# Optimization experiments

Hardware: AMD Instinct MI355X
Metric: run time of the kernel (lower is better)

The kernel has to match this reference:

```python
import jax, jax.numpy as jnp
import numpy as np

N, E, IN, H = 20000, 50000, 32, 64


def _lin_init(k, fan_in, shape):
    b = 1.0 / np.sqrt(fan_in)
    return jax.random.uniform(k, shape, jnp.float32, -b, b)


def setup_inputs() -> dict:
    key = jax.random.key(0)
    ks = jax.random.split(key, 16)
    inp = {
        "x": jax.random.normal(ks[0], (N, IN), jnp.float32),
        "edge_index": jax.random.randint(ks[1], (2, E), 0, N, dtype=jnp.int32),
        "edge_attr": jax.random.normal(ks[2], (E, 1, 2), jnp.float32),
        # layer 0: edge MLP 2->H->IN*H, root [IN,H], bias [H]
        "w1_0": _lin_init(ks[3], 2, (2, H)),
        "b1_0": _lin_init(ks[4], 2, (H,)),
        "w2_0": _lin_init(ks[5], H, (H, IN * H)),
        "b2_0": _lin_init(ks[6], H, (IN * H,)),
        "root_0": _lin_init(ks[7], IN, (IN, H)),
        "bias_0": _lin_init(ks[8], IN, (H,)),
        # layer 1: edge MLP 2->H->H*H, root [H,H], bias [H]
        "w1_1": _lin_init(ks[9], 2, (2, H)),
        "b1_1": _lin_init(ks[10], 2, (H,)),
        "w2_1": _lin_init(ks[11], H, (H, H * H)),
        "b2_1": _lin_init(ks[12], H, (H * H,)),
        "root_1": _lin_init(ks[13], H, (H, H)),
        "bias_1": _lin_init(ks[14], H, (H,)),
    }
    return inp


def _nnconv(x, src, dst, ea, w1, b1, w2, b2, root, bias, in_c, out_c):
    # per-edge weight matrices from edge-attr MLP: [E, in_c*out_c]
    h = jax.nn.relu(ea @ w1 + b1) @ w2 + b2
    W = h.reshape(-1, in_c, out_c)                     # [E, in, out]
    msg = jnp.einsum('ei,eio->eo', x[src], W)          # gather + per-edge matmul
    agg = jax.ops.segment_sum(msg, dst, num_segments=x.shape[0])  # scatter-add
    return agg + x @ root + bias                       # add aggr (PyG NNConv, aggr='add')


def reference(x, edge_index, edge_attr,
              w1_0, b1_0, w2_0, b2_0, root_0, bias_0,
              w1_1, b1_1, w2_1, b2_1, root_1, bias_1):
    src, dst = edge_index[0], edge_index[1]
    ea = edge_attr.reshape(edge_attr.shape[0], 2)      # [E, 2]
    x = jax.nn.relu(_nnconv(x, src, dst, ea, w1_0, b1_0, w2_0, b2_0, root_0, bias_0, IN, H))
    x = jax.nn.relu(_nnconv(x, src, dst, ea, w1_1, b1_1, w2_1, b2_1, root_1, bias_1, H, H))
    return x
```

## Files before the change

### kernel.cpp

```cpp
#include <hip/hip_runtime.h>

typedef _Float16 v8h __attribute__((ext_vector_type(8)));
typedef float v16f __attribute__((ext_vector_type(16)));

__global__ void prep_fused(const float* __restrict__ w2_0, const float* __restrict__ b2_0,
                           _Float16* __restrict__ BF0,
                           const float* __restrict__ w2_1, const float* __restrict__ b2_1,
                           _Float16* __restrict__ BF1,
                           const float* __restrict__ x, const float* __restrict__ root,
                           const float* __restrict__ bias, float* __restrict__ agg,
                           _Float16* __restrict__ xb, int N) {
    int idx = blockIdx.x * 256 + threadIdx.x;
    const int n0 = 264 * 512;
    const int n1 = 528 * 512;
    if (idx < n0 + n1) {
        const float* w2; const float* b2; _Float16* BF; int IN, rel;
        if (idx < n0) { w2 = w2_0; b2 = b2_0; BF = BF0; IN = 32; rel = idx; }
        else          { w2 = w2_1; b2 = b2_1; BF = BF1; IN = 64; rel = idx - n0; }
        int j = rel & 7, lane = (rel >> 3) & 63, f = rel >> 9;
        int nf = f & 1, kk16 = f >> 1;
        int ln = lane & 31, g2 = lane >> 5;
        int k = kk16 * 16 + g2 * 8 + j;
        int ko = k / IN, i = k - ko * IN;
        int o = nf * 32 + ln;
        float v = (ko < 64) ? w2[ko * (IN * 64) + i * 64 + o]
                : (ko == 64 ? b2[i * 64 + o] : 0.f);
        BF[rel] = (_Float16)v;
        return;
    }
    idx -= (n0 + n1);
    if (idx >= N * 64) return;
    int n = idx >> 6, o = idx & 63;
    float s = bias[o];
    const float* xr = x + (size_t)n * 32;
    #pragma unroll 8
    for (int i = 0; i < 32; ++i) s += xr[i] * root[i * 64 + o];
    agg[idx] = s;
    if (o < 32) xb[n * 32 + o] = (_Float16)xr[o];
}

__global__ void mid_kernel(const float* __restrict__ agg0, const float* __restrict__ root1,
                           const float* __restrict__ bias1, _Float16* __restrict__ x1b,
                           float* __restrict__ agg1, int N) {
    int idx = blockIdx.x * 256 + threadIdx.x;
    if (idx >= N * 64) return;
    int n = idx >> 6, o = idx & 63;
    const float* ar = agg0 + (size_t)n * 64;
    float s = bias1[o];
    #pragma unroll 8
    for (int i = 0; i < 64; ++i) s += fmaxf(ar[i], 0.f) * root1[i * 64 + o];
    agg1[idx] = s;
    x1b[idx] = (_Float16)fmaxf(agg0[idx], 0.f);
}

__global__ void final_relu(const float* __restrict__ agg1, float* __restrict__ out, int n) {
    int idx = blockIdx.x * 256 + threadIdx.x;
    if (idx < n) out[idx] = fmaxf(agg1[idx], 0.f);
}

template<int IN_C>
__global__ __launch_bounds__(512, 1)
void edge_gemm(const float* __restrict__ ea,
               const float* __restrict__ w1, const float* __restrict__ b1,
               const _Float16* __restrict__ xb, const _Float16* __restrict__ BF,
               const int* __restrict__ srcI, const int* __restrict__ dstI,
               float* __restrict__ agg, int E) {
    constexpr int PH  = IN_C / 16;
    constexpr int CPR = IN_C / 8;
    constexpr int M   = 256;
    constexpr int NCH = M * CPR;

    __shared__ __align__(16) uint4 sh_xf[NCH];
    __shared__ _Float16 sh_r1[M][66];
    __shared__ int sh_dst[M];

    int tid = threadIdx.x;
    int ebase = blockIdx.x * M;
    int valid = E - ebase; if (valid > M) valid = M;

    if (tid < M) {
        sh_dst[tid] = (tid < valid) ? dstI[ebase + tid] : 0;
        sh_r1[tid][64] = (_Float16)1.f;
    }
    for (int i = tid; i < M * 64; i += 512) {
        int e = i >> 6, j = i & 63;
        int ge = (e < valid) ? (ebase + e) : ebase;
        float2 av = *(const float2*)(ea + (size_t)ge * 2);
        sh_r1[e][j] = (_Float16)fmaxf(av.x * w1[j] + av.y * w1[64 + j] + b1[j], 0.f);
    }
    for (int d = tid; d < NCH; d += 512) {
        int ln = d & 31, g2 = (d >> 5) & 1;
        int sp = d >> 6;
        int p = sp & (PH - 1), s = sp / PH;
        int r = s * 32 + ln;
        int c = p * 2 + g2;
        int sidx = (r < valid) ? srcI[ebase + r] : 0;
        sh_xf[d] = *(const uint4*)(xb + (size_t)sidx * IN_C + (size_t)c * 8);
    }
    __syncthreads();

    int wv = tid >> 6, lane = tid & 63, ln = lane & 31, g2 = lane >> 5;
    int nf = wv & 1, q = wv >> 1;
    int sg0 = q * 2, sg1 = q * 2 + 1;

    v8h xs0[PH], xs1[PH];
    #pragma unroll
    for (int p = 0; p < PH; ++p) {
        xs0[p] = *(const v8h*)&sh_xf[((sg0 * PH + p) * 2 + g2) * 32 + ln];
        xs1[p] = *(const v8h*)&sh_xf[((sg1 * PH + p) * 2 + g2) * 32 + ln];
    }

    v16f acc0 = {0,0,0,0,0,0,0,0,0,0,0,0,0,0,0,0};
    v16f acc1 = acc0;

    const uint4* bp = (const uint4*)BF + (size_t)nf * 64 + lane;

    uint4 b[PH], bn[PH];
    auto LD = [&](uint4 (&d)[PH], int ko) {
        #pragma unroll
        for (int p = 0; p < PH; ++p) d[p] = bp[(size_t)(ko * PH + p) * 128];
    };
    auto FM = [&](uint4 (&d)[PH], int ko) {
        _Float16 sv0 = sh_r1[sg0 * 32 + ln][ko];
        _Float16 sv1 = sh_r1[sg1 * 32 + ln][ko];
        #pragma unroll
        for (int p = 0; p < PH; ++p) {
            v8h bb; __builtin_memcpy(&bb, &d[p], 16);
            acc0 = __builtin_amdgcn_mfma_f32_32x32x16_f16(xs0[p] * sv0, bb, acc0, 0, 0, 0);
            acc1 = __builtin_amdgcn_mfma_f32_32x32x16_f16(xs1[p] * sv1, bb, acc1, 0, 0, 0);
        }
    };

    LD(b, 0);
    #pragma unroll 1
    for (int t = 0; t < 32; ++t) {
        LD(bn, 2 * t + 1);
        FM(b,  2 * t);
        LD(b,  2 * t + 2);
        FM(bn, 2 * t + 1);
    }
    FM(b, 64);

    int colb = nf * 32 + ln;
    #pragma unroll
    for (int r = 0; r < 16; ++r) {
        int row = q * 64 + 4 * g2 + (r & 3) + 8 * (r >> 2);
        if (row < valid)
            atomicAdd(&agg[(size_t)sh_dst[row] * 64 + colb], acc0[r]);
        int row1 = row + 32;
        if (row1 < valid)
            atomicAdd(&agg[(size_t)sh_dst[row1] * 64 + colb], acc1[r]);
    }
}

extern "C" void kernel_launch(void* const* d_in, const int* in_sizes, int n_in,
                              void* d_out, int out_size, void* d_ws, size_t ws_size,
                              hipStream_t stream) {
    const float* x      = (const float*)d_in[0];
    const int*   ei     = (const int*)d_in[1];
    const float* ea     = (const float*)d_in[2];
    const float* w1_0   = (const float*)d_in[3];
    const float* b1_0   = (const float*)d_in[4];
    const float* w2_0   = (const float*)d_in[5];
    const float* b2_0   = (const float*)d_in[6];
    const float* root_0 = (const float*)d_in[7];
    const float* bias_0 = (const float*)d_in[8];
    const float* w1_1   = (const float*)d_in[9];
    const float* b1_1   = (const float*)d_in[10];
    const float* w2_1   = (const float*)d_in[11];
    const float* b2_1   = (const float*)d_in[12];
    const float* root_1 = (const float*)d_in[13];
    const float* bias_1 = (const float*)d_in[14];
    float* out = (float*)d_out;

    int N = in_sizes[0] / 32;
    int E = in_sizes[1] / 2;
    const int* srcI = ei;
    const int* dstI = ei + E;

    char* ws = (char*)d_ws;
    size_t off = 0;
    auto carve = [&](size_t bytes) {
        void* p = ws + off;
        off += (bytes + 255) & ~(size_t)255;
        return p;
    };
    _Float16* BF0  = (_Float16*)carve((size_t)264 * 512 * 2);
    _Float16* BF1  = (_Float16*)carve((size_t)528 * 512 * 2);
    _Float16* XB0  = (_Float16*)carve((size_t)N * 32 * 2);
    _Float16* X1B  = (_Float16*)carve((size_t)N * 64 * 2);
    float*    AGG0 = (float*)carve((size_t)N * 64 * 4);
    float*    AGG1 = (float*)carve((size_t)N * 64 * 4);

    int tprep = (264 + 528) * 512 + N * 64;
    prep_fused<<<(tprep + 255) / 256, 256, 0, stream>>>(w2_0, b2_0, BF0, w2_1, b2_1, BF1,
                                                        x, root_0, bias_0, AGG0, XB0, N);

    int gblocks = (E + 255) / 256;
    edge_gemm<32><<<gblocks, 512, 0, stream>>>(ea, w1_0, b1_0, XB0, BF0, srcI, dstI, AGG0, E);

    mid_kernel<<<(N * 64 + 255) / 256, 256, 0, stream>>>(AGG0, root_1, bias_1, X1B, AGG1, N);

    edge_gemm<64><<<gblocks, 512, 0, stream>>>(ea, w1_1, b1_1, X1B, BF1, srcI, dstI, AGG1, E);

    final_relu<<<(N * 64 + 255) / 256, 256, 0, stream>>>(AGG1, out, N * 64);
}
```

Measured before the change: 190.9 us.

## Drop shared-memory staging in edge GEMM; each wave owns one 32-edge tile

The edge GEMM no longer stages gathered source features, hidden activations and destination indices in LDS behind a block barrier. Each wave now handles 32 edges across both 32-column output halves. It computes its own edge-MLP hidden values in registers, gathers x rows directly from global memory, and loads both B fragments per step inside a fully unrolled 65-step loop. This removes the LDS traffic and the __syncthreads, and halves the A-side scaling per B fragment. In exchange, every wave now fetches twice as much of the shared B matrix per edge (B reuse across the two edge subgroups is lost), register pressure rises, and the explicit double-buffered prefetch is replaced by whatever the compiler schedules.

```diff
diff --git a/kernel.cpp b/kernel.cpp
--- a/kernel.cpp
+++ b/kernel.cpp
@@ -65,91 +65,70 @@
                const _Float16* __restrict__ xb, const _Float16* __restrict__ BF,
                const int* __restrict__ srcI, const int* __restrict__ dstI,
                float* __restrict__ agg, int E) {
-    constexpr int PH  = IN_C / 16;
-    constexpr int CPR = IN_C / 8;
-    constexpr int M   = 256;
-    constexpr int NCH = M * CPR;
+    constexpr int PH = IN_C / 16;
+    constexpr int M  = 256;
 
-    __shared__ __align__(16) uint4 sh_xf[NCH];
-    __shared__ _Float16 sh_r1[M][66];
-    __shared__ int sh_dst[M];
-
-    int tid = threadIdx.x;
+    int tid  = threadIdx.x;
+    int wv   = tid >> 6, lane = tid & 63, ln = lane & 31, g2 = lane >> 5;
+    int q    = wv;
     int ebase = blockIdx.x * M;
     int valid = E - ebase; if (valid > M) valid = M;
 
-    if (tid < M) {
-        sh_dst[tid] = (tid < valid) ? dstI[ebase + tid] : 0;
-        sh_r1[tid][64] = (_Float16)1.f;
+    int e  = q * 32 + ln;
+    int ge = (e < valid) ? (ebase + e) : ebase;
+
+    float a0 = ea[(size_t)ge * 2], a1 = ea[(size_t)ge * 2 + 1];
+    v8h sv[9];
+    #pragma unroll
+    for (int c = 0; c < 8; ++c) {
+        #pragma unroll
+        for (int j = 0; j < 8; ++j) {
+            int o = c * 8 + j;
+            float h = fmaf(a0, w1[o], fmaf(a1, w1[64 + o], b1[o]));
+            sv[c][j] = (_Float16)fmaxf(h, 0.f);
+        }
     }
-    for (int i = tid; i < M * 64; i += 512) {
-        int e = i >> 6, j = i & 63;
-        int ge = (e < valid) ? (ebase + e) : ebase;
-        float2 av = *(const float2*)(ea + (size_t)ge * 2);
-        sh_r1[e][j] = (_Float16)fmaxf(av.x * w1[j] + av.y * w1[64 + j] + b1[j], 0.f);
-    }
-    for (int d = tid; d < NCH; d += 512) {
-        int ln = d & 31, g2 = (d >> 5) & 1;
-        int sp = d >> 6;
-        int p = sp & (PH - 1), s = sp / PH;
-        int r = s * 32 + ln;
-        int c = p * 2 + g2;
-        int sidx = (r < valid) ? srcI[ebase + r] : 0;
-        sh_xf[d] = *(const uint4*)(xb + (size_t)sidx * IN_C + (size_t)c * 8);
-    }
-    __syncthreads();
+    #pragma unroll
+    for (int j = 0; j < 8; ++j) sv[8][j] = (_Float16)0.f;
+    sv[8][0] = (_Float16)1.f;
 
-    int wv = tid >> 6, lane = tid & 63, ln = lane & 31, g2 = lane >> 5;
-    int nf = wv & 1, q = wv >> 1;
-    int sg0 = q * 2, sg1 = q * 2 + 1;
-
-    v8h xs0[PH], xs1[PH];
+    int sidx = (e < valid) ? srcI[ebase + e] : 0;
+    const _Float16* xr = xb + (size_t)sidx * IN_C;
+    v8h xs[PH];
     #pragma unroll
-    for (int p = 0; p < PH; ++p) {
-        xs0[p] = *(const v8h*)&sh_xf[((sg0 * PH + p) * 2 + g2) * 32 + ln];
-        xs1[p] = *(const v8h*)&sh_xf[((sg1 * PH + p) * 2 + g2) * 32 + ln];
-    }
+    for (int p = 0; p < PH; ++p)
+        xs[p] = *(const v8h*)(xr + p * 16 + g2 * 8);
 
     v16f acc0 = {0,0,0,0,0,0,0,0,0,0,0,0,0,0,0,0};
     v16f acc1 = acc0;
 
-    const uint4* bp = (const uint4*)BF + (size_t)nf * 64 + lane;
+    const uint4* bp = (const uint4*)BF + lane;
 
-    uint4 b[PH], bn[PH];
-    auto LD = [&](uint4 (&d)[PH], int ko) {
-        #pragma unroll
-        for (int p = 0; p < PH; ++p) d[p] = bp[(size_t)(ko * PH + p) * 128];
-    };
-    auto FM = [&](uint4 (&d)[PH], int ko) {
-        _Float16 sv0 = sh_r1[sg0 * 32 + ln][ko];
-        _Float16 sv1 = sh_r1[sg1 * 32 + ln][ko];
+    #pragma unroll
+    for (int ko = 0; ko < 65; ++ko) {
+        _Float16 s = sv[ko >> 3][ko & 7];
         #pragma unroll
         for (int p = 0; p < PH; ++p) {
-            v8h bb; __builtin_memcpy(&bb, &d[p], 16);
-            acc0 = __builtin_amdgcn_mfma_f32_32x32x16_f16(xs0[p] * sv0, bb, acc0, 0, 0, 0);
-            acc1 = __builtin_amdgcn_mfma_f32_32x32x16_f16(xs1[p] * sv1, bb, acc1, 0, 0, 0);
+            v8h a = xs[p] * s;
+            uint4 u0 = bp[(size_t)(ko * PH + p) * 128];
+            uint4 u1 = bp[(size_t)(ko * PH + p) * 128 + 64];
+            v8h b0, b1v;
+            __builtin_memcpy(&b0, &u0, 16);
+            __builtin_memcpy(&b1v, &u1, 16);
+            acc0 = __builtin_amdgcn_mfma_f32_32x32x16_f16(a, b0, acc0, 0, 0, 0);
+            acc1 = __builtin_amdgcn_mfma_f32_32x32x16_f16(a, b1v, acc1, 0, 0, 0);
         }
-    };
+    }
 
-    LD(b, 0);
-    #pragma unroll 1
-    for (int t = 0; t < 32; ++t) {
-        LD(bn, 2 * t + 1);
-        FM(b,  2 * t);
-        LD(b,  2 * t + 2);
-        FM(bn, 2 * t + 1);
-    }
-    FM(b, 64);
-
-    int colb = nf * 32 + ln;
     #pragma unroll
     for (int r = 0; r < 16; ++r) {
-        int row = q * 64 + 4 * g2 + (r & 3) + 8 * (r >> 2);
-        if (row < valid)
-            atomicAdd(&agg[(size_t)sh_dst[row] * 64 + colb], acc0[r]);
-        int row1 = row + 32;
-        if (row1 < valid)
-            atomicAdd(&agg[(size_t)sh_dst[row1] * 64 + colb], acc1[r]);
+        int rr = 4 * g2 + (r & 3) + 8 * (r >> 2);
+        int er = q * 32 + rr;
+        if (er < valid) {
+            int d = dstI[ebase + er];
+            atomicAdd(&agg[(size_t)d * 64 + ln],      acc0[r]);
+            atomicAdd(&agg[(size_t)d * 64 + 32 + ln], acc1[r]);
+        }
     }
 }
 
```

New measurement: 212.3 us. +11.3%, slower.

## Stage edge-weight B fragments through double-buffered LDS chunks

Applied to the files above, without the earlier changes.

Rather than having each wave load the B (w2-derived) fragments straight from global memory into registers, the block now cooperatively loads chunks of several ko slices into a double-buffered shared-memory area. The next chunk is prefetched into registers while MFMAs run on the current one. The aim is to cut redundant global/L2 traffic, since the four waves sharing nf no longer each fetch the same B data. In exchange it adds a __syncthreads per chunk and extra LDS use, which may reduce overlap. The destination-index shared array is removed and dstI is read directly from global memory in the atomic epilogue.

```diff
diff --git a/kernel.cpp b/kernel.cpp
--- a/kernel.cpp
+++ b/kernel.cpp
@@ -65,22 +65,45 @@
                const _Float16* __restrict__ xb, const _Float16* __restrict__ BF,
                const int* __restrict__ srcI, const int* __restrict__ dstI,
                float* __restrict__ agg, int E) {
-    constexpr int PH  = IN_C / 16;
-    constexpr int CPR = IN_C / 8;
-    constexpr int M   = 256;
-    constexpr int NCH = M * CPR;
-
-    __shared__ __align__(16) uint4 sh_xf[NCH];
+    constexpr int PH   = IN_C / 16;
+    constexpr int CPR  = IN_C / 8;
+    constexpr int M    = 256;
+    constexpr int NCHX = M * CPR;
+    constexpr int KOB  = PH * 2 * 64 * 16;
+    constexpr int CK   = (IN_C == 64) ? 4 : 8;
+    constexpr int CHB  = CK * KOB;
+    constexpr int CHU4 = CHB / 16;
+    constexpr int NFULL = 64 / CK;
+    constexpr int NCHUNK = NFULL + 1;
+
+    __shared__ __align__(16) uint4 sh_b[2][CHU4];
+    __shared__ __align__(16) uint4 sh_xf[NCHX];
     __shared__ _Float16 sh_r1[M][66];
-    __shared__ int sh_dst[M];
 
     int tid = threadIdx.x;
     int ebase = blockIdx.x * M;
     int valid = E - ebase; if (valid > M) valid = M;
 
+    uint4 st[4];
+    auto LDG = [&](int t) {
+        int bytes = (t == NFULL) ? KOB : CHB;
+        const uint4* src = (const uint4*)BF + (size_t)t * CHU4 + tid;
+        #pragma unroll
+        for (int r = 0; r < 4; ++r)
+            if (tid * 16 + r * 8192 < bytes) st[r] = src[r * 512];
+    };
+    auto STW = [&](int cur, int t) {
+        int bytes = (t == NFULL) ? KOB : CHB;
+        #pragma unroll
+        for (int r = 0; r < 4; ++r)
+            if (tid * 16 + r * 8192 < bytes) sh_b[cur][r * 512 + tid] = st[r];
+    };
+
+    LDG(0);
+
     if (tid < M) {
-        sh_dst[tid] = (tid < valid) ? dstI[ebase + tid] : 0;
         sh_r1[tid][64] = (_Float16)1.f;
+        sh_r1[tid][65] = (_Float16)0.f;
     }
     for (int i = tid; i < M * 64; i += 512) {
         int e = i >> 6, j = i & 63;
@@ -88,20 +111,23 @@
         float2 av = *(const float2*)(ea + (size_t)ge * 2);
         sh_r1[e][j] = (_Float16)fmaxf(av.x * w1[j] + av.y * w1[64 + j] + b1[j], 0.f);
     }
-    for (int d = tid; d < NCH; d += 512) {
-        int ln = d & 31, g2 = (d >> 5) & 1;
+    for (int d = tid; d < NCHX; d += 512) {
+        int ln_ = d & 31, g2_ = (d >> 5) & 1;
         int sp = d >> 6;
         int p = sp & (PH - 1), s = sp / PH;
-        int r = s * 32 + ln;
-        int c = p * 2 + g2;
+        int r = s * 32 + ln_;
+        int c = p * 2 + g2_;
         int sidx = (r < valid) ? srcI[ebase + r] : 0;
         sh_xf[d] = *(const uint4*)(xb + (size_t)sidx * IN_C + (size_t)c * 8);
     }
+    STW(0, 0);
     __syncthreads();
 
     int wv = tid >> 6, lane = tid & 63, ln = lane & 31, g2 = lane >> 5;
-    int nf = wv & 1, q = wv >> 1;
-    int sg0 = q * 2, sg1 = q * 2 + 1;
+    int nf = wv & 1, mg = wv >> 1;
+    int sg0 = mg * 2, sg1 = mg * 2 + 1;
+    int e0 = sg0 * 32 + ln, e1 = sg1 * 32 + ln;
+    int nf64l = nf * 64 + lane;
 
     v8h xs0[PH], xs1[PH];
     #pragma unroll
@@ -113,43 +139,39 @@
     v16f acc0 = {0,0,0,0,0,0,0,0,0,0,0,0,0,0,0,0};
     v16f acc1 = acc0;
 
-    const uint4* bp = (const uint4*)BF + (size_t)nf * 64 + lane;
-
-    uint4 b[PH], bn[PH];
-    auto LD = [&](uint4 (&d)[PH], int ko) {
-        #pragma unroll
-        for (int p = 0; p < PH; ++p) d[p] = bp[(size_t)(ko * PH + p) * 128];
-    };
-    auto FM = [&](uint4 (&d)[PH], int ko) {
-        _Float16 sv0 = sh_r1[sg0 * 32 + ln][ko];
-        _Float16 sv1 = sh_r1[sg1 * 32 + ln][ko];
-        #pragma unroll
-        for (int p = 0; p < PH; ++p) {
-            v8h bb; __builtin_memcpy(&bb, &d[p], 16);
-            acc0 = __builtin_amdgcn_mfma_f32_32x32x16_f16(xs0[p] * sv0, bb, acc0, 0, 0, 0);
-            acc1 = __builtin_amdgcn_mfma_f32_32x32x16_f16(xs1[p] * sv1, bb, acc1, 0, 0, 0);
+    int cur = 0;
+    #pragma unroll 1
+    for (int t = 0; t < NCHUNK; ++t) {
+        if (t + 1 < NCHUNK) LDG(t + 1);
+        int cnt = (t == NFULL) ? 1 : CK;
+        #pragma unroll 1
+        for (int rel = 0; rel < cnt; ++rel) {
+            int ko = t * CK + rel;
+            _Float16 sv0 = sh_r1[e0][ko];
+            _Float16 sv1 = sh_r1[e1][ko];
+            #pragma unroll
+            for (int p = 0; p < PH; ++p) {
+                uint4 u = sh_b[cur][(rel * PH + p) * 128 + nf64l];
+                v8h bb; __builtin_memcpy(&bb, &u, 16);
+                acc0 = __builtin_amdgcn_mfma_f32_32x32x16_f16(xs0[p] * sv0, bb, acc0, 0, 0, 0);
+                acc1 = __builtin_amdgcn_mfma_f32_32x32x16_f16(xs1[p] * sv1, bb, acc1, 0, 0, 0);
+            }
         }
-    };
-
-    LD(b, 0);
-    #pragma unroll 1
-    for (int t = 0; t < 32; ++t) {
-        LD(bn, 2 * t + 1);
-        FM(b,  2 * t);
-        LD(b,  2 * t + 2);
-        FM(bn, 2 * t + 1);
-    }
-    FM(b, 64);
+        if (t + 1 < NCHUNK) STW(cur ^ 1, t + 1);
+        __syncthreads();
+        cur ^= 1;
+    }
 
     int colb = nf * 32 + ln;
     #pragma unroll
     for (int r = 0; r < 16; ++r) {
-        int row = q * 64 + 4 * g2 + (r & 3) + 8 * (r >> 2);
-        if (row < valid)
-            atomicAdd(&agg[(size_t)sh_dst[row] * 64 + colb], acc0[r]);
-        int row1 = row + 32;
-        if (row1 < valid)
-            atomicAdd(&agg[(size_t)sh_dst[row1] * 64 + colb], acc1[r]);
+        int rr = 4 * g2 + (r & 3) + 8 * (r >> 2);
+        int er0 = mg * 64 + rr;
+        if (er0 < valid)
+            atomicAdd(&agg[(size_t)dstI[ebase + er0] * 64 + colb], acc0[r]);
+        int er1 = er0 + 32;
+        if (er1 < valid)
+            atomicAdd(&agg[(size_t)dstI[ebase + er1] * 64 + colb], acc1[r]);
     }
 }
 
```

Measured after the change: 252.1 us. 1.32x slower.
